# Kernel tuning notes

Hardware: AMD Instinct MI355X
Metric: run time of the kernel (lower is better)

Reference implementation:

```python
import jax, jax.numpy as jnp
import numpy as np

B, S, D_IN, D_OUT = 4, 2048, 4096, 4096


def setup_inputs() -> dict:
    key = jax.random.key(0)
    k_x, k_w, k_s, k_z, k_b = jax.random.split(key, 5)
    x = jax.random.normal(k_x, (B, S, D_IN), dtype=jnp.float32)
    # int8 weight codes stored as int32 (values in [-128, 127])
    weight = jax.random.randint(k_w, (D_OUT, D_IN), -128, 128, dtype=jnp.int32)
    # per-output-channel quantization params
    scale = jax.random.uniform(k_s, (D_OUT, 1), dtype=jnp.float32, minval=0.005, maxval=0.02)
    zero_point = jax.random.uniform(k_z, (D_OUT, 1), dtype=jnp.float32, minval=-2.0, maxval=2.0)
    bias = jax.random.normal(k_b, (D_OUT,), dtype=jnp.float32)
    return {"x": x, "weight": weight, "scale": scale, "zero_point": zero_point, "bias": bias}


def reference(x, weight, scale, zero_point, bias):
    # Dequantize: w_fp = (int8_codes - zero_point) * scale  -> [D_OUT, D_IN]
    w_fp = (weight.astype(jnp.float32) - zero_point) * scale
    # F.linear: out = x @ w_fp.T + bias
    out = jnp.einsum("bsi,oi->bso", x, w_fp) + bias
    return out
```

## Files before the change

kernel.cpp:

```cpp
#include <hip/hip_runtime.h>
#include <hip/hip_bf16.h>

typedef int  i32x4 __attribute__((ext_vector_type(4)));

__global__ __launch_bounds__(256) void prep_fused(const float* __restrict__ x,
                                                  const int* __restrict__ w,
                                                  int* __restrict__ xq,
                                                  int* __restrict__ wq,
                                                  float* __restrict__ rsum,
                                                  float* __restrict__ rscale,
                                                  int M, int K) {
    if ((int)blockIdx.x >= M) {
        const size_t i = (size_t)(blockIdx.x - M) * blockDim.x + threadIdx.x;
        const int4* src = reinterpret_cast<const int4*>(w) + i * 4;
        int4 a = src[0], b = src[1], c = src[2], d = src[3];
        int4 o;
        o.x = (a.x & 255) | ((a.y & 255) << 8) | ((a.z & 255) << 16) | ((a.w & 255) << 24);
        o.y = (b.x & 255) | ((b.y & 255) << 8) | ((b.z & 255) << 16) | ((b.w & 255) << 24);
        o.z = (c.x & 255) | ((c.y & 255) << 8) | ((c.z & 255) << 16) | ((c.w & 255) << 24);
        o.w = (d.x & 255) | ((d.y & 255) << 8) | ((d.z & 255) << 16) | ((d.w & 255) << 24);
        reinterpret_cast<int4*>(wq)[i] = o;
        return;
    }
    const int row = blockIdx.x;
    const float* xr = x + (size_t)row * K;
    __shared__ float xs[4096];
    float mx = 0.f;
    for (int c = threadIdx.x * 4; c < K; c += blockDim.x * 4) {
        float4 v = *reinterpret_cast<const float4*>(xr + c);
        *reinterpret_cast<float4*>(xs + c) = v;
        mx = fmaxf(mx, fmaxf(fmaxf(fabsf(v.x), fabsf(v.y)),
                             fmaxf(fabsf(v.z), fabsf(v.w))));
    }
    #pragma unroll
    for (int off = 32; off > 0; off >>= 1) mx = fmaxf(mx, __shfl_down(mx, off));
    __shared__ float wmax[4];
    __shared__ float s_sx, s_inv;
    const int lane = threadIdx.x & 63, wv = threadIdx.x >> 6;
    if (lane == 0) wmax[wv] = mx;
    __syncthreads();
    if (threadIdx.x == 0) {
        float m = fmaxf(fmaxf(wmax[0], wmax[1]), fmaxf(wmax[2], wmax[3]));
        m = fmaxf(m, 1e-20f);
        s_sx = m / 127.f; s_inv = 127.f / m;
    }
    __syncthreads();
    const float inv = s_inv;
    int qs = 0;
    for (int c = threadIdx.x * 4; c < K; c += blockDim.x * 4) {
        float4 v = *reinterpret_cast<const float4*>(xs + c);
        const int q0 = __float2int_rn(v.x * inv), q1 = __float2int_rn(v.y * inv);
        const int q2 = __float2int_rn(v.z * inv), q3 = __float2int_rn(v.w * inv);
        qs += q0 + q1 + q2 + q3;
        const unsigned p = (unsigned)(q0 & 255) | ((unsigned)(q1 & 255) << 8) |
                           ((unsigned)(q2 & 255) << 16) | ((unsigned)(q3 & 255) << 24);
        xq[((size_t)row * K + c) >> 2] = (int)p;
    }
    #pragma unroll
    for (int off = 32; off > 0; off >>= 1) qs += __shfl_down(qs, off);
    __shared__ int wqs[4];
    if (lane == 0) wqs[wv] = qs;
    __syncthreads();
    if (threadIdx.x == 0) {
        const int t = wqs[0] + wqs[1] + wqs[2] + wqs[3];
        rsum[row] = s_sx * (float)t;
        rscale[row] = s_sx;
    }
}

__device__ __forceinline__ void async16(void* lds, const void* g) {
    __builtin_amdgcn_global_load_lds(
        (const __attribute__((address_space(1))) unsigned*)g,
        (__attribute__((address_space(3))) unsigned*)lds, 16, 0, 0);
}

__global__ __launch_bounds__(512, 2) void qgemm1p(
    const char* __restrict__ A, const char* __restrict__ B,
    const float* __restrict__ rsum, const float* __restrict__ rscale,
    const float* __restrict__ scale, const float* __restrict__ zp,
    const float* __restrict__ bias, float* __restrict__ C,
    int M, int N, int K) {
    extern __shared__ char smem[];
    char* const AsB = smem;
    char* const BsB = smem + 65536;

    const int tid  = threadIdx.x;
    const int lane = tid & 63;
    const int wid  = tid >> 6;
    const int wm = wid >> 2, wn = wid & 3;
    const int l15 = lane & 15;

    const int nbn = N >> 8;
    int wg = blockIdx.x;
    wg = (wg & 7) * (gridDim.x >> 3) + (wg >> 3);
    const int bm = wg / nbn, bn = wg % nbn;

    const int r0s = tid >> 2, sls = tid & 3;
    size_t a_src[2], b_src[2];
    int lds_off[2];
    #pragma unroll
    for (int j = 0; j < 2; ++j) {
        const int row = r0s + j * 128;
        const int sl  = sls ^ ((row >> 1) & 3);
        a_src[j] = ((size_t)(bm * 256 + row)) * K + sl * 16;
        b_src[j] = ((size_t)(bn * 256 + row)) * K + sl * 16;
        lds_off[j] = (j * 512 + tid) * 16;
    }

    auto STAGE = [&](int u, int sl) {
        const int kc = u * 64;
        char* const da = AsB + sl * 16384;
        char* const db = BsB + sl * 16384;
        #pragma unroll
        for (int j = 0; j < 2; ++j) async16(da + lds_off[j], A + a_src[j] + kc);
        #pragma unroll
        for (int j = 0; j < 2; ++j) async16(db + lds_off[j], B + b_src[j] + kc);
    };

    const int sw16 = (((lane >> 4) ^ ((lane >> 1) & 3)) << 4);
    const int a_ro = (wm * 128 + l15) * 64 + sw16;
    const int b_ro = (wn * 64 + l15) * 64 + sw16;

    i32x4 acc[8][4] = {};

    const int NS = K >> 6;

#define PHASE(S, SL)                                                           \
    {                                                                          \
        const char* _ha = AsB + (SL) * 16384;                                  \
        const char* _hb = BsB + (SL) * 16384;                                  \
        i32x4 af[8], bf[4];                                                    \
        _Pragma("unroll")                                                      \
        for (int m = 0; m < 8; ++m)                                            \
            af[m] = *(const i32x4*)(_ha + a_ro + m * 1024);                    \
        _Pragma("unroll")                                                      \
        for (int n = 0; n < 4; ++n)                                            \
            bf[n] = *(const i32x4*)(_hb + b_ro + n * 1024);                    \
        int _u = (S) + 3; if (_u >= NS) _u = NS - 1;                           \
        STAGE(_u, ((SL) + 3) & 3);                                             \
        asm volatile("s_waitcnt lgkmcnt(0)" ::: "memory");                     \
        __builtin_amdgcn_sched_barrier(0);                                     \
        __builtin_amdgcn_s_setprio(1);                                         \
        _Pragma("unroll")                                                      \
        for (int m = 0; m < 8; ++m)                                            \
            _Pragma("unroll")                                                  \
            for (int n = 0; n < 4; ++n)                                        \
                acc[m][n] = __builtin_amdgcn_mfma_i32_16x16x64_i8(             \
                    af[m], bf[n], acc[m][n], 0, 0, 0);                         \
        __builtin_amdgcn_s_setprio(0);                                         \
        __builtin_amdgcn_sched_barrier(0);                                     \
        asm volatile("s_waitcnt vmcnt(4)" ::: "memory");                       \
        asm volatile("s_barrier" ::: "memory");                                \
    }

    STAGE(0, 0); STAGE(1, 1); STAGE(2, 2);
    asm volatile("s_waitcnt vmcnt(8)" ::: "memory");
    asm volatile("s_barrier" ::: "memory");

    #pragma unroll 1
    for (int i = 0; i < NS / 4; ++i) {
        const int s = 4 * i;
        PHASE(s + 0, 0)
        PHASE(s + 1, 1)
        PHASE(s + 2, 2)
        PHASE(s + 3, 3)
    }
#undef PHASE

    float sc[4], zz[4], bb[4];
    #pragma unroll
    for (int n = 0; n < 4; ++n) {
        const int o = bn * 256 + wn * 64 + n * 16 + l15;
        sc[n] = scale[o]; zz[n] = zp[o]; bb[n] = bias[o];
    }
    const int hi4 = (lane >> 4) << 2;
    #pragma unroll
    for (int mf = 0; mf < 8; ++mf) {
        const int r0 = bm * 256 + wm * 128 + mf * 16 + hi4;
        float rs[4], sx[4];
        #pragma unroll
        for (int i = 0; i < 4; ++i) { rs[i] = rsum[r0 + i]; sx[i] = rscale[r0 + i]; }
        #pragma unroll
        for (int n = 0; n < 4; ++n) {
            const int o = bn * 256 + wn * 64 + n * 16 + l15;
            #pragma unroll
            for (int i = 0; i < 4; ++i)
                C[(size_t)(r0 + i) * N + o] =
                    sc[n] * (sx[i] * (float)acc[mf][n][i] - zz[n] * rs[i]) + bb[n];
        }
    }
}

extern "C" void kernel_launch(void* const* d_in, const int* in_sizes, int n_in,
                              void* d_out, int out_size, void* d_ws, size_t ws_size,
                              hipStream_t stream) {
    const float* x     = (const float*)d_in[0];
    const int*   w     = (const int*)d_in[1];
    const float* scale = (const float*)d_in[2];
    const float* zp    = (const float*)d_in[3];
    const float* bias  = (const float*)d_in[4];
    float* out = (float*)d_out;

    const int N = in_sizes[2];
    const int K = in_sizes[1] / N;
    const int M = in_sizes[0] / K;

    char*  xq  = (char*)d_ws;
    char*  wq  = (char*)d_ws + (size_t)M * K;
    float* rs  = (float*)((char*)d_ws + (size_t)M * K + (size_t)N * K);
    float* rsc = rs + M;

    const int wblocks = (int)(((size_t)N * K / 16) / 256);
    prep_fused<<<M + wblocks, 256, 0, stream>>>(x, w, (int*)xq, (int*)wq,
                                                rs, rsc, M, K);

    (void)hipFuncSetAttribute((const void*)qgemm1p,
                              hipFuncAttributeMaxDynamicSharedMemorySize, 131072);
    const int nwg = (M / 256) * (N / 256);
    qgemm1p<<<nwg, 512, 131072, stream>>>(xq, wq, rs, rsc, scale, zp, bias,
                                          out, M, N, K);
}
```

Baseline: 178.5 us.

## Load B fragments directly from global into double-buffered registers, bypassing LDS

```diff
diff --git a/kernel.cpp b/kernel.cpp
--- a/kernel.cpp
+++ b/kernel.cpp
@@ -74,7 +74,14 @@
         (__attribute__((address_space(3))) unsigned*)lds, 16, 0, 0);
 }
 
-__global__ __launch_bounds__(512, 2) void qgemm1p(
+__device__ __forceinline__ i32x4 gload16(const void* p) {
+    i32x4 r;
+    asm volatile("global_load_dwordx4 %0, %1, off"
+                 : "=&v"(r) : "v"(p) : "memory");
+    return r;
+}
+
+__global__ __launch_bounds__(512, 2) void qgemmbd(
     const char* __restrict__ A, const char* __restrict__ B,
     const float* __restrict__ rsum, const float* __restrict__ rscale,
     const float* __restrict__ scale, const float* __restrict__ zp,
@@ -82,7 +89,6 @@
     int M, int N, int K) {
     extern __shared__ char smem[];
     char* const AsB = smem;
-    char* const BsB = smem + 65536;
 
     const int tid  = threadIdx.x;
     const int lane = tid & 63;
@@ -96,48 +102,55 @@
     const int bm = wg / nbn, bn = wg % nbn;
 
     const int r0s = tid >> 2, sls = tid & 3;
-    size_t a_src[2], b_src[2];
+    size_t a_src[2];
     int lds_off[2];
     #pragma unroll
     for (int j = 0; j < 2; ++j) {
         const int row = r0s + j * 128;
         const int sl  = sls ^ ((row >> 1) & 3);
         a_src[j] = ((size_t)(bm * 256 + row)) * K + sl * 16;
-        b_src[j] = ((size_t)(bn * 256 + row)) * K + sl * 16;
         lds_off[j] = (j * 512 + tid) * 16;
     }
 
-    auto STAGE = [&](int u, int sl) {
+    auto AST = [&](int u, int sl) {
         const int kc = u * 64;
         char* const da = AsB + sl * 16384;
-        char* const db = BsB + sl * 16384;
         #pragma unroll
         for (int j = 0; j < 2; ++j) async16(da + lds_off[j], A + a_src[j] + kc);
-        #pragma unroll
-        for (int j = 0; j < 2; ++j) async16(db + lds_off[j], B + b_src[j] + kc);
     };
+
+    const char* bp[4];
+    #pragma unroll
+    for (int n = 0; n < 4; ++n)
+        bp[n] = B + ((size_t)(bn * 256 + wn * 64 + n * 16 + l15)) * K
+                  + ((lane >> 4) << 4);
 
     const int sw16 = (((lane >> 4) ^ ((lane >> 1) & 3)) << 4);
     const int a_ro = (wm * 128 + l15) * 64 + sw16;
-    const int b_ro = (wn * 64 + l15) * 64 + sw16;
 
     i32x4 acc[8][4] = {};
+    i32x4 bfX[4], bfY[4];
 
     const int NS = K >> 6;
 
-#define PHASE(S, SL)                                                           \
+#define BLOAD(DST, U)                                                          \
+    {                                                                          \
+        _Pragma("unroll")                                                      \
+        for (int n = 0; n < 4; ++n)                                            \
+            DST[n] = gload16(bp[n] + ((size_t)(U) << 6));                      \
+    }
+
+#define PHASE(S, SL, BUSE, BNXT)                                               \
     {                                                                          \
         const char* _ha = AsB + (SL) * 16384;                                  \
-        const char* _hb = BsB + (SL) * 16384;                                  \
-        i32x4 af[8], bf[4];                                                    \
+        i32x4 af[8];                                                           \
         _Pragma("unroll")                                                      \
         for (int m = 0; m < 8; ++m)                                            \
             af[m] = *(const i32x4*)(_ha + a_ro + m * 1024);                    \
-        _Pragma("unroll")                                                      \
-        for (int n = 0; n < 4; ++n)                                            \
-            bf[n] = *(const i32x4*)(_hb + b_ro + n * 1024);                    \
-        int _u = (S) + 3; if (_u >= NS) _u = NS - 1;                           \
-        STAGE(_u, ((SL) + 3) & 3);                                             \
+        int _u1 = (S) + 1; if (_u1 >= NS) _u1 = NS - 1;                        \
+        BLOAD(BNXT, _u1)                                                       \
+        int _u3 = (S) + 3; if (_u3 >= NS) _u3 = NS - 1;                        \
+        AST(_u3, ((SL) + 3) & 3);                                              \
         asm volatile("s_waitcnt lgkmcnt(0)" ::: "memory");                     \
         __builtin_amdgcn_sched_barrier(0);                                     \
         __builtin_amdgcn_s_setprio(1);                                         \
@@ -146,26 +159,28 @@
             _Pragma("unroll")                                                  \
             for (int n = 0; n < 4; ++n)                                        \
                 acc[m][n] = __builtin_amdgcn_mfma_i32_16x16x64_i8(             \
-                    af[m], bf[n], acc[m][n], 0, 0, 0);                         \
+                    af[m], BUSE[n], acc[m][n], 0, 0, 0);                       \
         __builtin_amdgcn_s_setprio(0);                                         \
         __builtin_amdgcn_sched_barrier(0);                                     \
-        asm volatile("s_waitcnt vmcnt(4)" ::: "memory");                       \
+        asm volatile("s_waitcnt vmcnt(2)" ::: "memory");                       \
         asm volatile("s_barrier" ::: "memory");                                \
     }
 
-    STAGE(0, 0); STAGE(1, 1); STAGE(2, 2);
-    asm volatile("s_waitcnt vmcnt(8)" ::: "memory");
+    AST(0, 0); AST(1, 1); AST(2, 2);
+    BLOAD(bfX, 0)
+    asm volatile("s_waitcnt vmcnt(0)" ::: "memory");
     asm volatile("s_barrier" ::: "memory");
 
     #pragma unroll 1
     for (int i = 0; i < NS / 4; ++i) {
         const int s = 4 * i;
-        PHASE(s + 0, 0)
-        PHASE(s + 1, 1)
-        PHASE(s + 2, 2)
-        PHASE(s + 3, 3)
+        PHASE(s + 0, 0, bfX, bfY)
+        PHASE(s + 1, 1, bfY, bfX)
+        PHASE(s + 2, 2, bfX, bfY)
+        PHASE(s + 3, 3, bfY, bfX)
     }
 #undef PHASE
+#undef BLOAD
 
     float sc[4], zz[4], bb[4];
     #pragma unroll
@@ -214,9 +229,9 @@
     prep_fused<<<M + wblocks, 256, 0, stream>>>(x, w, (int*)xq, (int*)wq,
                                                 rs, rsc, M, K);
 
-    (void)hipFuncSetAttribute((const void*)qgemm1p,
-                              hipFuncAttributeMaxDynamicSharedMemorySize, 131072);
+    (void)hipFuncSetAttribute((const void*)qgemmbd,
+                              hipFuncAttributeMaxDynamicSharedMemorySize, 65536);
     const int nwg = (M / 256) * (N / 256);
-    qgemm1p<<<nwg, 512, 131072, stream>>>(xq, wq, rs, rsc, scale, zp, bias,
-                                          out, M, N, K);
-}
+    qgemmbd<<<nwg, 512, 65536, stream>>>(xq, wq, rs, rsc, scale, zp, bias,
+                                         out, M, N, K);
+}
```

Measured after the change: 233.9 us. +31.1%, slower.
